# Performance work log

Measured on AMD Instinct MI355X. Metric: run time of the kernel, lower is better.

The kernel has to match this reference:

```python
import jax, jax.numpy as jnp
import numpy as np

EPS = 1e-6
ROPE_BASE = 10000.0


def rmsnorm(x, w):
    xf = x.astype(jnp.float32)
    var = jnp.mean(xf * xf, axis=-1, keepdims=True)
    return (w * (xf * jax.lax.rsqrt(var + EPS))).astype(x.dtype)


def rotate_half(x):
    h = x.shape[-1] // 2
    return jnp.concatenate([-x[..., h:], x[..., :h]], axis=-1)


def setup_inputs() -> dict:
    key = jax.random.key(0)
    ks = jax.random.split(key, 10)
    B, S, H, nH, nKV, hd, I = 2, 2048, 2048, 16, 4, 128, 8192
    hidden_states = jax.random.normal(ks[0], (B, S, H), dtype=jnp.float32)
    # additive causal mask, broadcast over batch/heads
    causal = jnp.triu(jnp.full((S, S), -1e9, dtype=jnp.float32), k=1)
    attention_mask = causal[None, None]  # [1,1,S,S]
    position_ids = jnp.broadcast_to(jnp.arange(S, dtype=jnp.int64), (B, S))
    s = 0.02
    return {
        'hidden_states': hidden_states,
        'attention_mask': attention_mask,
        'position_ids': position_ids,
        'ln1_w': jnp.ones((H,), jnp.float32),
        'Wq': jax.random.normal(ks[1], (H, nH * hd), jnp.float32) * s,
        'Wk': jax.random.normal(ks[2], (H, nKV * hd), jnp.float32) * s,
        'Wv': jax.random.normal(ks[3], (H, nKV * hd), jnp.float32) * s,
        'Wo': jax.random.normal(ks[4], (nH * hd, H), jnp.float32) * s,
        'qn_w': jnp.ones((hd,), jnp.float32),
        'kn_w': jnp.ones((hd,), jnp.float32),
        'ln2_w': jnp.ones((H,), jnp.float32),
        'Wg': jax.random.normal(ks[5], (H, I), jnp.float32) * s,
        'Wu': jax.random.normal(ks[6], (H, I), jnp.float32) * s,
        'Wd': jax.random.normal(ks[7], (I, H), jnp.float32) * s,
    }


def reference(hidden_states, attention_mask, position_ids, ln1_w, Wq, Wk, Wv, Wo,
              qn_w, kn_w, ln2_w, Wg, Wu, Wd):
    B, S, H = hidden_states.shape
    hd = qn_w.shape[0]
    nH = Wq.shape[1] // hd
    nKV = Wk.shape[1] // hd

    # --- attention block ---
    h = rmsnorm(hidden_states, ln1_w)
    q = (h @ Wq).reshape(B, S, nH, hd).transpose(0, 2, 1, 3)   # [B,nH,S,hd]
    k = (h @ Wk).reshape(B, S, nKV, hd).transpose(0, 2, 1, 3)  # [B,nKV,S,hd]
    v = (h @ Wv).reshape(B, S, nKV, hd).transpose(0, 2, 1, 3)

    # RoPE cache (fp32), gathered by position_ids
    inv_freq = 1.0 / (ROPE_BASE ** (jnp.arange(0, hd, 2, dtype=jnp.float32) / hd))
    freqs = jnp.outer(jnp.arange(S, dtype=jnp.float32), inv_freq)
    emb = jnp.concatenate([freqs, freqs], axis=-1)  # [S,hd]
    cos = jnp.cos(emb)[position_ids][:, None]  # [B,1,S,hd]
    sin = jnp.sin(emb)[position_ids][:, None]
    q = q * cos + rotate_half(q) * sin
    k = k * cos + rotate_half(k) * sin

    # QK RMSNorm after RoPE
    q = rmsnorm(q, qn_w)
    k = rmsnorm(k, kn_w)

    # GQA broadcast
    rep = nH // nKV
    k = jnp.repeat(k, rep, axis=1)
    v = jnp.repeat(v, rep, axis=1)

    scores = jnp.einsum('bhqd,bhkd->bhqk', q, k) / np.float32(np.sqrt(hd))
    scores = scores + attention_mask
    attn = jax.nn.softmax(scores.astype(jnp.float32), axis=-1).astype(q.dtype)
    out = jnp.einsum('bhqk,bhkd->bhqd', attn, v)
    out = out.transpose(0, 2, 1, 3).reshape(B, S, nH * hd)
    x = hidden_states + out @ Wo

    # --- MLP block (SwiGLU) ---
    h2 = rmsnorm(x, ln2_w)
    x = x + (jax.nn.silu(h2 @ Wg) * (h2 @ Wu)) @ Wd
    return x
```

## Files before the change

kernel.cpp:

```cpp
#include <hip/hip_runtime.h>
#include <math.h>

typedef __bf16 bf16;
typedef bf16 bf16x8 __attribute__((ext_vector_type(8)));
typedef float f32x4 __attribute__((ext_vector_type(4)));
typedef unsigned int uint32;

#define B_   2
#define S_   2048
#define H_   2048
#define NH_  16
#define NKV_ 4
#define HD_  128
#define I_   8192
#define M_   (B_ * S_)

typedef __attribute__((address_space(3))) void       lds_void;
typedef __attribute__((address_space(1))) const void gbl_void;

__device__ __forceinline__ void async16(const void* g, void* l) {
  __builtin_amdgcn_global_load_lds((gbl_void*)g, (lds_void*)l, 16, 0, 0);
}

__global__ void probe_k(const uint32* __restrict__ x, int* __restrict__ flag) {
  const int lane = threadIdx.x;
  const uint32 u = x[lane];
  float blo = fabsf(__uint_as_float(u << 16));
  float bhi = fabsf(__uint_as_float(u & 0xffff0000u));
  float fv  = fabsf(__uint_as_float(u));
  if (!(blo < 1e30f)) blo = 3e38f;
  if (!(bhi < 1e30f)) bhi = 3e38f;
  if (!(fv  < 1e30f)) fv  = 3e38f;
  float mb = fmaxf(blo, bhi);
  float mf = fv;
#pragma unroll
  for (int off = 1; off < 64; off <<= 1) {
    mb = fmaxf(mb, __shfl_xor(mb, off, 64));
    mf = fmaxf(mf, __shfl_xor(mf, off, 64));
  }
  if (lane == 0) *flag = (mf < mb) ? 1 : 0;
}

template <bool INRAW>
__global__ __launch_bounds__(256) void rmsnorm_k(const void* __restrict__ xin,
                                                 const void* __restrict__ w,
                                                 bf16* __restrict__ out,
                                                 const int* __restrict__ dtp) {
  const int f    = *dtp;
  const int row  = blockIdx.x;
  const int tid  = threadIdx.x;
  const int base = row * H_ + tid * 8;

  float v[8];
  if (INRAW && f) {
    const float* xf = (const float*)xin + base;
    f32x4 a = *(const f32x4*)xf, b = *(const f32x4*)(xf + 4);
#pragma unroll
    for (int i = 0; i < 4; ++i) { v[i] = a[i]; v[4 + i] = b[i]; }
  } else {
    bf16x8 t = *(const bf16x8*)((const bf16*)xin + base);
#pragma unroll
    for (int i = 0; i < 8; ++i) v[i] = (float)t[i];
  }

  float ss = 0.f;
#pragma unroll
  for (int i = 0; i < 8; ++i) ss += v[i] * v[i];
#pragma unroll
  for (int off = 1; off < 64; off <<= 1) ss += __shfl_xor(ss, off, 64);

  __shared__ float red[4];
  if ((tid & 63) == 0) red[tid >> 6] = ss;
  __syncthreads();
  ss = red[0] + red[1] + red[2] + red[3];

  const float scale = rsqrtf(ss * (1.0f / H_) + 1e-6f);
  float wv[8];
  if (f) {
    const float* wf = (const float*)w + tid * 8;
    f32x4 a = *(const f32x4*)wf, b = *(const f32x4*)(wf + 4);
#pragma unroll
    for (int i = 0; i < 4; ++i) { wv[i] = a[i]; wv[4 + i] = b[i]; }
  } else {
    bf16x8 t = *(const bf16x8*)((const bf16*)w + tid * 8);
#pragma unroll
    for (int i = 0; i < 8; ++i) wv[i] = (float)t[i];
  }
  bf16x8 o;
#pragma unroll
  for (int i = 0; i < 8; ++i) o[i] = (bf16)(wv[i] * (v[i] * scale));
  *(bf16x8*)(out + base) = o;
}

__global__ __launch_bounds__(256) void convert_wt(const void* __restrict__ W,
                                                  bf16* __restrict__ Wt,
                                                  const int K, const int N,
                                                  const int* __restrict__ dtp) {
  __shared__ bf16 sT[64][72];
  const int f   = *dtp;
  const int tid = threadIdx.x;
  const int k0  = blockIdx.y * 64;
  const int n0  = blockIdx.x * 64;
  if (f) {
#pragma unroll
    for (int p = 0; p < 4; ++p) {
      const int g  = tid + p * 256;
      const int r  = g >> 4;
      const int c4 = (g & 15) * 4;
      f32x4 v = *(const f32x4*)((const float*)W + (size_t)(k0 + r) * N + n0 + c4);
#pragma unroll
      for (int u = 0; u < 4; ++u) sT[c4 + u][r] = (bf16)v[u];
    }
  } else {
#pragma unroll
    for (int p = 0; p < 2; ++p) {
      const int g  = tid + p * 256;
      const int r  = g >> 3;
      const int c8 = (g & 7) * 8;
      bf16x8 v = *(const bf16x8*)((const bf16*)W + (size_t)(k0 + r) * N + n0 + c8);
#pragma unroll
      for (int u = 0; u < 8; ++u) sT[c8 + u][r] = v[u];
    }
  }
  __syncthreads();
#pragma unroll
  for (int p = 0; p < 2; ++p) {
    const int g  = tid + p * 256;
    const int n  = g >> 3;
    const int k8 = (g & 7) * 8;
    bf16x8 ov;
#pragma unroll
    for (int u = 0; u < 8; ++u) ov[u] = sT[n][k8 + u];
    *(bf16x8*)(Wt + (size_t)(n0 + n) * K + k0 + k8) = ov;
  }
}

#define BARX() do { asm volatile("" ::: "memory");                       \
                    __builtin_amdgcn_s_barrier();                        \
                    asm volatile("" ::: "memory"); } while (0)
#define VMW6() asm volatile("s_waitcnt vmcnt(6)" ::: "memory")

template <int EPI, bool AUXRAW, bool CRAW>
__global__ __launch_bounds__(512, 2) void gemm8_k(const bf16* __restrict__ A,
                                                  const bf16* __restrict__ Bt,
                                                  void* __restrict__ C,
                                                  const void* __restrict__ aux,
                                                  const int M, const int N,
                                                  const int K,
                                                  const int* __restrict__ dtp) {
  __shared__ __align__(16) bf16 sA[2][256][64];
  __shared__ __align__(16) bf16 sB[2][256][64];

  const int f    = *dtp;
  const int tid  = threadIdx.x;
  const int lane = tid & 63;
  const int wave = tid >> 6;
  const int wr   = wave >> 2;
  const int wc   = wave & 3;
  const int l15  = lane & 15;
  const int quad = lane >> 4;

  const int gx  = gridDim.x;
  const int nwg = gx * gridDim.y;
  int bid = blockIdx.y * gx + blockIdx.x;
  if ((nwg & 7) == 0) bid = (bid & 7) * (nwg >> 3) + (bid >> 3);
  const int row0 = (bid / gx) * 256;
  const int col0 = (bid % gx) * 256;

  const int NT = K >> 6;

  const int swo = (l15 & 7) << 4;
  const int cb0 = (quad * 16) ^ swo;
  const int cb1 = (64 + quad * 16) ^ swo;
  char* sAc = (char*)&sA[0][0][0];
  char* sBc = (char*)&sB[0][0][0];

  const int d0   = tid * 16;
  const int d1   = 8192 + tid * 16;
  const int p0   = d0 ^ (((d0 >> 7) & 7) << 4);
  const int p1   = d1 ^ (((d1 >> 7) & 7) << 4);
  const int rg0  = p0 >> 7, cbs0 = p0 & 127;
  const int rg1  = p1 >> 7, cbs1 = p1 & 127;
  const size_t K2 = (size_t)K * 2;
  const char* gA = (const char*)A  + (size_t)row0 * K2;
  const char* gB = (const char*)Bt + (size_t)col0 * K2;

#define STAGE8(gbase, sbase, s, h, t) do {                                     \
    const int tt_ = ((t) < NT) ? (t) : ((t) - NT);                             \
    const size_t go_ = (size_t)tt_ * 128;                                      \
    async16(gbase + (size_t)((h) * 128 + rg0) * K2 + go_ + cbs0,               \
            (sbase) + (s) * 32768 + (h) * 16384 + tid * 16);                   \
    async16(gbase + (size_t)((h) * 128 + rg1) * K2 + go_ + cbs1,               \
            (sbase) + (s) * 32768 + (h) * 16384 + 8192 + tid * 16);            \
  } while (0)
#define STA(s, h, t) STAGE8(gA, sAc, s, h, t)
#define STB(s, h, t) STAGE8(gB, sBc, s, h, t)

  bf16x8 af[4][2], bfr[2][2];
  f32x4 acc[8][4];
#pragma unroll
  for (int m = 0; m < 8; ++m)
#pragma unroll
    for (int n = 0; n < 4; ++n)
#pragma unroll
      for (int r = 0; r < 4; ++r) acc[m][n][r] = 0.f;

#define LDA8(s, mh) do {                                                       \
    _Pragma("unroll")                                                          \
    for (int mi = 0; mi < 4; ++mi) {                                           \
      const int rb = ((mh) * 128 + wr * 64 + mi * 16 + l15) * 128;             \
      af[mi][0] = *(const bf16x8*)(sAc + (s) * 32768 + rb + cb0);              \
      af[mi][1] = *(const bf16x8*)(sAc + (s) * 32768 + rb + cb1);              \
    }                                                                          \
  } while (0)

#define LDB8(s, nh) do {                                                       \
    _Pragma("unroll")                                                          \
    for (int ni = 0; ni < 2; ++ni) {                                           \
      const int rb = ((nh) * 128 + wc * 32 + ni * 16 + l15) * 128;             \
      bfr[ni][0] = *(const bf16x8*)(sBc + (s) * 32768 + rb + cb0);             \
      bfr[ni][1] = *(const bf16x8*)(sBc + (s) * 32768 + rb + cb1);             \
    }                                                                          \
  } while (0)

#define MFMA16(mh, nh) do {                                                    \
    __builtin_amdgcn_s_setprio(1);                                             \
    _Pragma("unroll")                                                          \
    for (int mi = 0; mi < 4; ++mi)                                             \
      _Pragma("unroll")                                                        \
      for (int ni = 0; ni < 2; ++ni) {                                         \
        acc[(mh)*4+mi][(nh)*2+ni] = __builtin_amdgcn_mfma_f32_16x16x32_bf16(   \
            af[mi][0], bfr[ni][0], acc[(mh)*4+mi][(nh)*2+ni], 0, 0, 0);        \
        acc[(mh)*4+mi][(nh)*2+ni] = __builtin_amdgcn_mfma_f32_16x16x32_bf16(   \
            af[mi][1], bfr[ni][1], acc[(mh)*4+mi][(nh)*2+ni], 0, 0, 0);        \
      }                                                                        \
    __builtin_amdgcn_s_setprio(0);                                             \
  } while (0)

  STA(0, 0, 0); STA(0, 1, 0); STB(0, 0, 0); STB(0, 1, 0);
  STA(1, 0, 1); STA(1, 1, 1); STB(1, 0, 1);
  VMW6();
  BARX();

#pragma unroll 1
  for (int T = 0; T < NT; T += 2) {
    LDA8(0, 0); LDB8(0, 0);
    STB(1, 1, T + 1);
    BARX(); MFMA16(0, 0); BARX();
    LDB8(0, 1);
    STA(0, 0, T + 2);
    BARX(); MFMA16(0, 1); BARX();
    LDA8(0, 1); LDB8(0, 0);
    BARX(); MFMA16(1, 0); BARX();
    LDB8(0, 1);
    STA(0, 1, T + 2); STB(0, 0, T + 2);
    BARX(); MFMA16(1, 1); VMW6(); BARX();
    LDA8(1, 0); LDB8(1, 0);
    STB(0, 1, T + 2);
    BARX(); MFMA16(0, 0); BARX();
    LDB8(1, 1);
    STA(1, 0, T + 3);
    BARX(); MFMA16(0, 1); BARX();
    LDA8(1, 1); LDB8(1, 0);
    BARX(); MFMA16(1, 0); BARX();
    LDB8(1, 1);
    STA(1, 1, T + 3); STB(1, 0, T + 3);
    BARX(); MFMA16(1, 1); VMW6(); BARX();
  }
  asm volatile("s_waitcnt vmcnt(0)" ::: "memory");

#pragma unroll
  for (int m = 0; m < 8; ++m) {
#pragma unroll
    for (int n = 0; n < 4; ++n) {
#pragma unroll
      for (int r = 0; r < 4; ++r) {
        const int row = row0 + (m >> 2) * 128 + wr * 64 + (m & 3) * 16 + quad * 4 + r;
        const int col = col0 + (n >> 1) * 128 + wc * 32 + (n & 1) * 16 + l15;
        const size_t idx = (size_t)row * N + col;
        const float val  = acc[m][n][r];
        float outv;
        if (EPI == 0) {
          outv = val;
        } else {
          const float av = (AUXRAW && f) ? ((const float*)aux)[idx]
                                         : (float)((const bf16*)aux)[idx];
          if (EPI == 1) {
            outv = val + av;
          } else {
            const float sg = av / (1.f + __expf(-av));
            outv = sg * val;
          }
        }
        if (CRAW && f) ((float*)C)[idx] = outv;
        else           ((bf16*)C)[idx]  = (bf16)outv;
      }
    }
  }
#undef STAGE8
#undef STA
#undef STB
#undef LDA8
#undef LDB8
#undef MFMA16
}

template <int EPI, bool AUXRAW, bool CRAW>
__global__ __launch_bounds__(256) void gemm_bt_k(const bf16* __restrict__ A,
                                                 const bf16* __restrict__ Bt,
                                                 void* __restrict__ C,
                                                 const void* __restrict__ aux,
                                                 const int M, const int N, const int K,
                                                 const int* __restrict__ dtp) {
  __shared__ __align__(16) bf16 sA[128][32];
  __shared__ __align__(16) bf16 sB[128][32];

  const int f    = *dtp;
  const int tid  = threadIdx.x;
  const int lane = tid & 63;
  const int wave = tid >> 6;
  const int wm   = (wave >> 1) * 64;
  const int wn   = (wave & 1) * 64;
  const int row0 = blockIdx.y * 128;
  const int col0 = blockIdx.x * 128;
  const int l15  = lane & 15;
  const int quad = lane >> 4;

  f32x4 acc[4][4];
#pragma unroll
  for (int i = 0; i < 4; ++i)
#pragma unroll
    for (int j = 0; j < 4; ++j)
#pragma unroll
      for (int r = 0; r < 4; ++r) acc[i][j][r] = 0.f;

  const int o  = tid * 16;
  const int r0 = o >> 6;
  const int ib = o & 63;

  const char* gA0 = (const char*)(A  + (size_t)(row0 + r0)      * K) + ib;
  const char* gA1 = (const char*)(A  + (size_t)(row0 + 64 + r0) * K) + ib;
  const char* gB0 = (const char*)(Bt + (size_t)(col0 + r0)      * K) + ib;
  const char* gB1 = (const char*)(Bt + (size_t)(col0 + 64 + r0) * K) + ib;
  char* lA = (char*)(&sA[0][0]) + wave * 1024;
  char* lB = (char*)(&sB[0][0]) + wave * 1024;

  for (int k0 = 0; k0 < K; k0 += 32) {
    async16(gA0, lA);
    async16(gA1, lA + 4096);
    async16(gB0, lB);
    async16(gB1, lB + 4096);
    gA0 += 64; gA1 += 64; gB0 += 64; gB1 += 64;
    __syncthreads();

    bf16x8 af[4], bfr[4];
#pragma unroll
    for (int i = 0; i < 4; ++i)
      af[i] = *(const bf16x8*)(&sA[wm + i * 16 + l15][quad * 8]);
#pragma unroll
    for (int j = 0; j < 4; ++j)
      bfr[j] = *(const bf16x8*)(&sB[wn + j * 16 + l15][quad * 8]);
#pragma unroll
    for (int i = 0; i < 4; ++i)
#pragma unroll
      for (int j = 0; j < 4; ++j)
        acc[i][j] = __builtin_amdgcn_mfma_f32_16x16x32_bf16(af[i], bfr[j],
                                                            acc[i][j], 0, 0, 0);
    __syncthreads();
  }

#pragma unroll
  for (int i = 0; i < 4; ++i) {
#pragma unroll
    for (int j = 0; j < 4; ++j) {
#pragma unroll
      for (int r = 0; r < 4; ++r) {
        const int row    = row0 + wm + i * 16 + quad * 4 + r;
        const int col    = col0 + wn + j * 16 + l15;
        const size_t idx = (size_t)row * N + col;
        const float val  = acc[i][j][r];
        float outv;
        if (EPI == 0) {
          outv = val;
        } else {
          const float av = (AUXRAW && f) ? ((const float*)aux)[idx]
                                         : (float)((const bf16*)aux)[idx];
          if (EPI == 1) {
            outv = val + av;
          } else {
            const float sg = av / (1.f + __expf(-av));
            outv = sg * val;
          }
        }
        if (CRAW && f) ((float*)C)[idx] = outv;
        else           ((bf16*)C)[idx]  = (bf16)outv;
      }
    }
  }
}

template <int EPI, bool AUXRAW, bool CRAW>
__global__ __launch_bounds__(256) void gemm_k(const bf16* __restrict__ A,
                                              const void* __restrict__ Bm,
                                              void* __restrict__ C,
                                              const void* __restrict__ aux,
                                              const int M, const int N, const int K,
                                              const int* __restrict__ dtp) {
  __shared__ __align__(16) bf16 sA[128][40];
  __shared__ __align__(16) bf16 sB[128][40];

  const int f    = *dtp;
  const int tid  = threadIdx.x;
  const int lane = tid & 63;
  const int wave = tid >> 6;
  const int wm   = (wave >> 1) * 64;
  const int wn   = (wave & 1) * 64;
  const int row0 = blockIdx.y * 128;
  const int col0 = blockIdx.x * 128;
  const int l15  = lane & 15;
  const int quad = lane >> 4;

  f32x4 acc[4][4];
#pragma unroll
  for (int i = 0; i < 4; ++i)
#pragma unroll
    for (int j = 0; j < 4; ++j)
#pragma unroll
      for (int r = 0; r < 4; ++r) acc[i][j][r] = 0.f;

  for (int k0 = 0; k0 < K; k0 += 32) {
#pragma unroll
    for (int pass = 0; pass < 2; ++pass) {
      const int g  = tid + pass * 256;
      const int ar = g >> 2, ac = (g & 3) * 8;
      *(bf16x8*)(&sA[ar][ac]) =
          *(const bf16x8*)(A + (size_t)(row0 + ar) * K + k0 + ac);
      const int br = g >> 4, bc = (g & 15) * 8;
      const size_t boff = (size_t)(k0 + br) * N + col0 + bc;
      bf16x8 bv;
      if (f) {
        const float* bp = (const float*)Bm + boff;
        f32x4 lo = *(const f32x4*)bp, hi = *(const f32x4*)(bp + 4);
#pragma unroll
        for (int u = 0; u < 8; ++u) bv[u] = (bf16)(u < 4 ? lo[u] : hi[u - 4]);
      } else {
        bv = *(const bf16x8*)((const bf16*)Bm + boff);
      }
#pragma unroll
      for (int u = 0; u < 8; ++u) sB[bc + u][br] = bv[u];
    }
    __syncthreads();

    bf16x8 af[4], bfr[4];
#pragma unroll
    for (int i = 0; i < 4; ++i)
      af[i] = *(const bf16x8*)(&sA[wm + i * 16 + l15][quad * 8]);
#pragma unroll
    for (int j = 0; j < 4; ++j)
      bfr[j] = *(const bf16x8*)(&sB[wn + j * 16 + l15][quad * 8]);
#pragma unroll
    for (int i = 0; i < 4; ++i)
#pragma unroll
      for (int j = 0; j < 4; ++j)
        acc[i][j] = __builtin_amdgcn_mfma_f32_16x16x32_bf16(af[i], bfr[j],
                                                            acc[i][j], 0, 0, 0);
    __syncthreads();
  }

#pragma unroll
  for (int i = 0; i < 4; ++i) {
#pragma unroll
    for (int j = 0; j < 4; ++j) {
#pragma unroll
      for (int r = 0; r < 4; ++r) {
        const int row    = row0 + wm + i * 16 + quad * 4 + r;
        const int col    = col0 + wn + j * 16 + l15;
        const size_t idx = (size_t)row * N + col;
        const float val  = acc[i][j][r];
        float outv;
        if (EPI == 0) {
          outv = val;
        } else {
          const float av = (AUXRAW && f) ? ((const float*)aux)[idx]
                                         : (float)((const bf16*)aux)[idx];
          if (EPI == 1) {
            outv = val + av;
          } else {
            const float sg = av / (1.f + __expf(-av));
            outv = sg * val;
          }
        }
        if (CRAW && f) ((float*)C)[idx] = outv;
        else           ((bf16*)C)[idx]  = (bf16)outv;
      }
    }
  }
}

__global__ __launch_bounds__(256) void rope_norm_k(bf16* __restrict__ q,
                                                   bf16* __restrict__ k,
                                                   const void* __restrict__ qw,
                                                   const void* __restrict__ kw,
                                                   const int* __restrict__ dtp) {
  const int f    = *dtp;
  const int task = blockIdx.x * 4 + (threadIdx.x >> 6);
  const int lane = threadIdx.x & 63;
  const int row  = task / 20;
  const int hh   = task - row * 20;

  bf16* p;
  const void* w;
  if (hh < NH_) { p = q + (size_t)row * 2048 + hh * 128;        w = qw; }
  else          { p = k + (size_t)row * 512 + (hh - NH_) * 128; w = kw; }

  const float pos = (float)(row & (S_ - 1));
  const float inv = powf(10000.f, -(float)lane * (1.f / 64.f));
  float sn, cs;
  sincosf(pos * inv, &sn, &cs);

  const float x0 = (float)p[lane], x1 = (float)p[lane + 64];
  const float r0 = x0 * cs - x1 * sn;
  const float r1 = x1 * cs + x0 * sn;

  float ss = r0 * r0 + r1 * r1;
#pragma unroll
  for (int off = 1; off < 64; off <<= 1) ss += __shfl_xor(ss, off, 64);
  const float scale = rsqrtf(ss * (1.f / 128.f) + 1e-6f);

  const float w0 = f ? ((const float*)w)[lane]      : (float)((const bf16*)w)[lane];
  const float w1 = f ? ((const float*)w)[lane + 64] : (float)((const bf16*)w)[lane + 64];
  p[lane]      = (bf16)(w0 * (r0 * scale));
  p[lane + 64] = (bf16)(w1 * (r1 * scale));
}

__global__ __launch_bounds__(256) void transpose_v(const bf16* __restrict__ v,
                                                   bf16* __restrict__ vt) {
  __shared__ bf16 sT[64][68];
  const int tid = threadIdx.x;
  const int r0  = blockIdx.y * 64;
  const int c0  = blockIdx.x * 64;
  const int b   = r0 >> 11;
  const int s0  = r0 & 2047;
#pragma unroll
  for (int p = 0; p < 2; ++p) {
    const int g   = tid + p * 256;
    const int row = g >> 3;
    const int c8  = (g & 7) * 8;
    bf16x8 tv = *(const bf16x8*)(v + (size_t)(r0 + row) * 512 + c0 + c8);
#pragma unroll
    for (int u = 0; u < 8; ++u) sT[c8 + u][row] = tv[u];
  }
  __syncthreads();
#pragma unroll
  for (int p = 0; p < 2; ++p) {
    const int g  = tid + p * 256;
    const int oc = g >> 3;
    const int s8 = (g & 7) * 8;
    bf16x8 ov;
#pragma unroll
    for (int u = 0; u < 8; ++u) ov[u] = sT[oc][s8 + u];
    *(bf16x8*)(vt + ((size_t)(b * 512 + c0 + oc)) * 2048 + s0 + s8) = ov;
  }
}

__global__ __launch_bounds__(256) void attn_mfma(const bf16* __restrict__ q,
                                                 const bf16* __restrict__ k,
                                                 const bf16* __restrict__ vt,
                                                 bf16* __restrict__ ctx) {
  __shared__ __align__(16) bf16 sK[64][136];
  __shared__ __align__(16) bf16 sV[128][72];
  __shared__ __align__(16) bf16 sP[4][16][72];

  const int tid  = threadIdx.x;
  const int lane = tid & 63;
  const int wave = tid >> 6;
  const int l15  = lane & 15;
  const int quad = lane >> 4;

  const int bid = blockIdx.x;
  const int i7  = bid & 127;
  const int qt  = (i7 & 1) ? (127 - (i7 >> 1)) : (i7 >> 1);
  const int kvh = (bid >> 7) & 3;
  const int b   = bid >> 9;
  const int q0  = qt * 16;
  const int h   = kvh * 4 + wave;

  bf16x8 qf[4];
  {
    const bf16* qp = q + (size_t)(b * S_ + q0 + l15) * 2048 + h * 128 + quad * 8;
#pragma unroll
    for (int c = 0; c < 4; ++c) qf[c] = *(const bf16x8*)(qp + c * 32);
  }

  float m4[4], l4[4];
  f32x4 of[8];
#pragma unroll
  for (int r = 0; r < 4; ++r) { m4[r] = -1e30f; l4[r] = 0.f; }
#pragma unroll
  for (int dg = 0; dg < 8; ++dg)
#pragma unroll
    for (int r = 0; r < 4; ++r) of[dg][r] = 0.f;

  const int ntiles = (q0 + 16 + 63) >> 6;
  const bf16* kbase = k + (size_t)b * S_ * 512 + kvh * 128;
  const bf16* vbase = vt + (size_t)(b * 512 + kvh * 128) * 2048;
  const float sc = 0.088388347648318447f;

  for (int t = 0; t < ntiles; ++t) {
    const int j0 = t << 6;
#pragma unroll
    for (int p = 0; p < 4; ++p) {
      const int g   = tid + p * 256;
      const int dc  = g & 15;
      const int key = g >> 4;
      *(bf16x8*)(&sK[key][dc * 8]) =
          *(const bf16x8*)(kbase + (size_t)(j0 + key) * 512 + dc * 8);
    }
#pragma unroll
    for (int p = 0; p < 4; ++p) {
      const int g   = tid + p * 256;
      const int dim = g >> 3;
      const int k8  = (g & 7) * 8;
      *(bf16x8*)(&sV[dim][k8]) =
          *(const bf16x8*)(vbase + (size_t)dim * 2048 + j0 + k8);
    }
    __syncthreads();

    f32x4 sa[4];
#pragma unroll
    for (int g = 0; g < 4; ++g)
#pragma unroll
      for (int r = 0; r < 4; ++r) sa[g][r] = 0.f;
#pragma unroll
    for (int g = 0; g < 4; ++g)
#pragma unroll
      for (int c = 0; c < 4; ++c) {
        bf16x8 kf = *(const bf16x8*)(&sK[g * 16 + l15][c * 32 + quad * 8]);
        sa[g] = __builtin_amdgcn_mfma_f32_16x16x32_bf16(qf[c], kf, sa[g], 0, 0, 0);
      }

    float s[4][4];
    const bool mask = (t == ntiles - 1);
#pragma unroll
    for (int g = 0; g < 4; ++g)
#pragma unroll
      for (int r = 0; r < 4; ++r) {
        float x = sa[g][r] * sc;
        if (mask && (j0 + g * 16 + l15 > q0 + quad * 4 + r)) x = -1e30f;
        s[g][r] = x;
      }

    float al[4];
#pragma unroll
    for (int r = 0; r < 4; ++r) {
      float rm = fmaxf(fmaxf(s[0][r], s[1][r]), fmaxf(s[2][r], s[3][r]));
#pragma unroll
      for (int off = 1; off < 16; off <<= 1) rm = fmaxf(rm, __shfl_xor(rm, off, 64));
      const float mn = fmaxf(m4[r], rm);
      al[r] = __expf(m4[r] - mn);
      float rs = 0.f;
#pragma unroll
      for (int g = 0; g < 4; ++g) { s[g][r] = __expf(s[g][r] - mn); rs += s[g][r]; }
#pragma unroll
      for (int off = 1; off < 16; off <<= 1) rs += __shfl_xor(rs, off, 64);
      l4[r] = l4[r] * al[r] + rs;
      m4[r] = mn;
    }
#pragma unroll
    for (int dg = 0; dg < 8; ++dg)
#pragma unroll
      for (int r = 0; r < 4; ++r) of[dg][r] *= al[r];

#pragma unroll
    for (int g = 0; g < 4; ++g)
#pragma unroll
      for (int r = 0; r < 4; ++r)
        sP[wave][quad * 4 + r][g * 16 + l15] = (bf16)s[g][r];
    bf16x8 pf[2];
#pragma unroll
    for (int c = 0; c < 2; ++c)
      pf[c] = *(const bf16x8*)(&sP[wave][l15][c * 32 + quad * 8]);

#pragma unroll
    for (int c = 0; c < 2; ++c)
#pragma unroll
      for (int dg = 0; dg < 8; ++dg) {
        bf16x8 vf = *(const bf16x8*)(&sV[dg * 16 + l15][c * 32 + quad * 8]);
        of[dg] = __builtin_amdgcn_mfma_f32_16x16x32_bf16(pf[c], vf, of[dg], 0, 0, 0);
      }
    __syncthreads();
  }

  bf16* op = ctx + (size_t)(b * S_ + q0) * 2048 + h * 128;
#pragma unroll
  for (int r = 0; r < 4; ++r) {
    const float rl = 1.f / l4[r];
    const int row  = quad * 4 + r;
#pragma unroll
    for (int dg = 0; dg < 8; ++dg)
      op[(size_t)row * 2048 + dg * 16 + l15] = (bf16)(of[dg][r] * rl);
  }
}

extern "C" void kernel_launch(void* const* d_in, const int* in_sizes, int n_in,
                              void* d_out, int out_size, void* d_ws, size_t ws_size,
                              hipStream_t stream) {
  (void)in_sizes; (void)n_in; (void)out_size;

  const void* hidden = d_in[0];
  const void* ln1 = d_in[3];
  const void* Wq  = d_in[4];
  const void* Wk  = d_in[5];
  const void* Wv  = d_in[6];
  const void* Wo  = d_in[7];
  const void* qn  = d_in[8];
  const void* kn  = d_in[9];
  const void* ln2 = d_in[10];
  const void* Wg  = d_in[11];
  const void* Wu  = d_in[12];
  const void* Wd  = d_in[13];

  int*  dtp   = (int*)d_ws;
  bf16* slotA = (bf16*)((char*)d_ws + 16);
  bf16* slotB = slotA + (size_t)M_ * 2048;
  bf16* slotC = slotB + (size_t)M_ * 2048;
  bf16* slotD = slotC + (size_t)M_ * 512;
  bf16* slotE = slotD + (size_t)M_ * 512;
  bf16* vT    = slotE;
  bf16* wT    = slotE + (size_t)M_ * 8192;

  const size_t need = 16 + 2ull * ((size_t)M_ * 2048 * 2 + (size_t)M_ * 512 * 2 +
                                   (size_t)M_ * 8192 + (size_t)I_ * H_);

  probe_k<<<1, 64, 0, stream>>>((const uint32*)hidden, dtp);
  rmsnorm_k<true><<<M_, 256, 0, stream>>>(hidden, ln1, slotA, dtp);

  if (ws_size >= need) {
    convert_wt<<<dim3(32, 32), 256, 0, stream>>>(Wq, wT, 2048, 2048, dtp);
    gemm8_k<0, false, false><<<dim3(8, 16), 512, 0, stream>>>(slotA, wT, slotB, nullptr, M_, 2048, 2048, dtp);
    convert_wt<<<dim3(8, 32), 256, 0, stream>>>(Wk, wT, 2048, 512, dtp);
    gemm_bt_k<0, false, false><<<dim3(4, 32), 256, 0, stream>>>(slotA, wT, slotC, nullptr, M_, 512, 2048, dtp);
    convert_wt<<<dim3(8, 32), 256, 0, stream>>>(Wv, wT, 2048, 512, dtp);
    gemm_bt_k<0, false, false><<<dim3(4, 32), 256, 0, stream>>>(slotA, wT, slotD, nullptr, M_, 512, 2048, dtp);
    transpose_v<<<dim3(8, 64), 256, 0, stream>>>(slotD, vT);
    rope_norm_k<<<(M_ * (NH_ + NKV_)) / 4, 256, 0, stream>>>(slotB, slotC, qn, kn, dtp);
    attn_mfma<<<B_ * NKV_ * (S_ / 16), 256, 0, stream>>>(slotB, slotC, vT, slotA);
    convert_wt<<<dim3(32, 32), 256, 0, stream>>>(Wo, wT, 2048, 2048, dtp);
    gemm8_k<1, true, false><<<dim3(8, 16), 512, 0, stream>>>(slotA, wT, slotB, hidden, M_, 2048, 2048, dtp);
    rmsnorm_k<false><<<M_, 256, 0, stream>>>(slotB, ln2, slotA, dtp);
    convert_wt<<<dim3(128, 32), 256, 0, stream>>>(Wg, wT, 2048, 8192, dtp);
    gemm8_k<0, false, false><<<dim3(32, 16), 512, 0, stream>>>(slotA, wT, slotE, nullptr, M_, 8192, 2048, dtp);
    convert_wt<<<dim3(128, 32), 256, 0, stream>>>(Wu, wT, 2048, 8192, dtp);
    gemm8_k<2, false, false><<<dim3(32, 16), 512, 0, stream>>>(slotA, wT, slotE, slotE, M_, 8192, 2048, dtp);
    convert_wt<<<dim3(32, 128), 256, 0, stream>>>(Wd, wT, 8192, 2048, dtp);
    gemm8_k<1, false, true><<<dim3(8, 16), 512, 0, stream>>>(slotE, wT, d_out, slotB, M_, 2048, 8192, dtp);
  } else {
    gemm_k<0, false, false><<<dim3(16, 32), 256, 0, stream>>>(slotA, Wq, slotB, nullptr, M_, 2048, 2048, dtp);
    gemm_k<0, false, false><<<dim3(4, 32), 256, 0, stream>>>(slotA, Wk, slotC, nullptr, M_, 512, 2048, dtp);
    gemm_k<0, false, false><<<dim3(4, 32), 256, 0, stream>>>(slotA, Wv, slotD, nullptr, M_, 512, 2048, dtp);
    transpose_v<<<dim3(8, 64), 256, 0, stream>>>(slotD, vT);
    rope_norm_k<<<(M_ * (NH_ + NKV_)) / 4, 256, 0, stream>>>(slotB, slotC, qn, kn, dtp);
    attn_mfma<<<B_ * NKV_ * (S_ / 16), 256, 0, stream>>>(slotB, slotC, vT, slotA);
    gemm_k<1, true, false><<<dim3(16, 32), 256, 0, stream>>>(slotA, Wo, slotB, hidden, M_, 2048, 2048, dtp);
    rmsnorm_k<false><<<M_, 256, 0, stream>>>(slotB, ln2, slotA, dtp);
    gemm_k<0, false, false><<<dim3(64, 32), 256, 0, stream>>>(slotA, Wg, slotE, nullptr, M_, 8192, 2048, dtp);
    gemm_k<2, false, false><<<dim3(64, 32), 256, 0, stream>>>(slotA, Wu, slotE, slotE, M_, 8192, 2048, dtp);
    gemm_k<1, false, true><<<dim3(16, 32), 256, 0, stream>>>(slotE, Wd, d_out, slotB, M_, 2048, 8192, dtp);
  }
}
```

Measured before the change: 1.420 ms.

## Split-K the narrow GEMMs into two partials and add a combine kernel

The Q/K/V, O and down-projection GEMMs now run with split-K across blockIdx.z. Each half writes fp32 partials to extra workspace, and a new combine kernel sums the halves and applies the residual/epilogue. This doubles the workgroup count for the 128-tile GEMMs, which underfill the GPU, at the cost of extra fp32 partial traffic and additional launches. The gemm8 barrier macro also drops its compiler fences, and an explicit lgkmcnt(0) wait with a sched_barrier is added before each MFMA block. The new path only runs when the workspace is large enough; otherwise the previous path is kept.

```diff
diff --git a/kernel.cpp b/kernel.cpp
--- a/kernel.cpp
+++ b/kernel.cpp
@@ -3,6 +3,7 @@
 
 typedef __bf16 bf16;
 typedef bf16 bf16x8 __attribute__((ext_vector_type(8)));
+typedef bf16 bf16x4 __attribute__((ext_vector_type(4)));
 typedef float f32x4 __attribute__((ext_vector_type(4)));
 typedef unsigned int uint32;
 
@@ -135,10 +136,58 @@
   }
 }
 
-#define BARX() do { asm volatile("" ::: "memory");                       \
-                    __builtin_amdgcn_s_barrier();                        \
-                    asm volatile("" ::: "memory"); } while (0)
-#define VMW6() asm volatile("s_waitcnt vmcnt(6)" ::: "memory")
+template <int EPI, bool AUXRAW, bool CRAW>
+__global__ __launch_bounds__(256) void combine_k(const float* __restrict__ p0,
+                                                 const float* __restrict__ p1,
+                                                 const void* __restrict__ aux,
+                                                 void* __restrict__ C,
+                                                 const size_t total,
+                                                 const int* __restrict__ dtp) {
+  const int f = *dtp;
+  const size_t i = ((size_t)blockIdx.x * 256 + threadIdx.x) * 4;
+  if (i >= total) return;
+  f32x4 a = *(const f32x4*)(p0 + i);
+  f32x4 b = *(const f32x4*)(p1 + i);
+  float av4[4];
+  if (EPI != 0) {
+    if (AUXRAW && f) {
+      f32x4 t = *(const f32x4*)((const float*)aux + i);
+#pragma unroll
+      for (int u = 0; u < 4; ++u) av4[u] = t[u];
+    } else {
+      bf16x4 t = *(const bf16x4*)((const bf16*)aux + i);
+#pragma unroll
+      for (int u = 0; u < 4; ++u) av4[u] = (float)t[u];
+    }
+  }
+  float o[4];
+#pragma unroll
+  for (int u = 0; u < 4; ++u) {
+    const float val = a[u] + b[u];
+    if (EPI == 0) o[u] = val;
+    else if (EPI == 1) o[u] = val + av4[u];
+    else {
+      const float sg = av4[u] / (1.f + __expf(-av4[u]));
+      o[u] = sg * val;
+    }
+  }
+  if (CRAW && f) {
+    f32x4 ov; 
+#pragma unroll
+    for (int u = 0; u < 4; ++u) ov[u] = o[u];
+    *(f32x4*)((float*)C + i) = ov;
+  } else {
+    bf16x4 ov;
+#pragma unroll
+    for (int u = 0; u < 4; ++u) ov[u] = (bf16)o[u];
+    *(bf16x4*)((bf16*)C + i) = ov;
+  }
+}
+
+#define BARX()  __builtin_amdgcn_s_barrier()
+#define LGKM0() do { asm volatile("s_waitcnt lgkmcnt(0)" ::: "memory");       \
+                     __builtin_amdgcn_sched_barrier(0); } while (0)
+#define VMW6()  asm volatile("s_waitcnt vmcnt(6)" ::: "memory")
 
 template <int EPI, bool AUXRAW, bool CRAW>
 __global__ __launch_bounds__(512, 2) void gemm8_k(const bf16* __restrict__ A,
@@ -146,7 +195,7 @@
                                                   void* __restrict__ C,
                                                   const void* __restrict__ aux,
                                                   const int M, const int N,
-                                                  const int K,
+                                                  const int K, const int lda,
                                                   const int* __restrict__ dtp) {
   __shared__ __align__(16) bf16 sA[2][256][64];
   __shared__ __align__(16) bf16 sB[2][256][64];
@@ -166,6 +215,7 @@
   if ((nwg & 7) == 0) bid = (bid & 7) * (nwg >> 3) + (bid >> 3);
   const int row0 = (bid / gx) * 256;
   const int col0 = (bid % gx) * 256;
+  const int koff = blockIdx.z * K;
 
   const int NT = K >> 6;
 
@@ -181,16 +231,16 @@
   const int p1   = d1 ^ (((d1 >> 7) & 7) << 4);
   const int rg0  = p0 >> 7, cbs0 = p0 & 127;
   const int rg1  = p1 >> 7, cbs1 = p1 & 127;
-  const size_t K2 = (size_t)K * 2;
-  const char* gA = (const char*)A  + (size_t)row0 * K2;
-  const char* gB = (const char*)Bt + (size_t)col0 * K2;
+  const size_t LD2 = (size_t)lda * 2;
+  const char* gA = (const char*)A  + (size_t)row0 * LD2 + (size_t)koff * 2;
+  const char* gB = (const char*)Bt + (size_t)col0 * LD2 + (size_t)koff * 2;
 
 #define STAGE8(gbase, sbase, s, h, t) do {                                     \
     const int tt_ = ((t) < NT) ? (t) : ((t) - NT);                             \
     const size_t go_ = (size_t)tt_ * 128;                                      \
-    async16(gbase + (size_t)((h) * 128 + rg0) * K2 + go_ + cbs0,               \
+    async16(gbase + (size_t)((h) * 128 + rg0) * LD2 + go_ + cbs0,              \
             (sbase) + (s) * 32768 + (h) * 16384 + tid * 16);                   \
-    async16(gbase + (size_t)((h) * 128 + rg1) * K2 + go_ + cbs1,               \
+    async16(gbase + (size_t)((h) * 128 + rg1) * LD2 + go_ + cbs1,              \
             (sbase) + (s) * 32768 + (h) * 16384 + 8192 + tid * 16);            \
   } while (0)
 #define STA(s, h, t) STAGE8(gA, sAc, s, h, t)
@@ -246,29 +296,31 @@
   for (int T = 0; T < NT; T += 2) {
     LDA8(0, 0); LDB8(0, 0);
     STB(1, 1, T + 1);
-    BARX(); MFMA16(0, 0); BARX();
+    BARX(); LGKM0(); MFMA16(0, 0); BARX();
     LDB8(0, 1);
     STA(0, 0, T + 2);
-    BARX(); MFMA16(0, 1); BARX();
+    BARX(); LGKM0(); MFMA16(0, 1); BARX();
     LDA8(0, 1); LDB8(0, 0);
-    BARX(); MFMA16(1, 0); BARX();
+    BARX(); LGKM0(); MFMA16(1, 0); BARX();
     LDB8(0, 1);
     STA(0, 1, T + 2); STB(0, 0, T + 2);
-    BARX(); MFMA16(1, 1); VMW6(); BARX();
+    BARX(); LGKM0(); MFMA16(1, 1); VMW6(); BARX();
     LDA8(1, 0); LDB8(1, 0);
     STB(0, 1, T + 2);
-    BARX(); MFMA16(0, 0); BARX();
+    BARX(); LGKM0(); MFMA16(0, 0); BARX();
     LDB8(1, 1);
     STA(1, 0, T + 3);
-    BARX(); MFMA16(0, 1); BARX();
+    BARX(); LGKM0(); MFMA16(0, 1); BARX();
     LDA8(1, 1); LDB8(1, 0);
-    BARX(); MFMA16(1, 0); BARX();
+    BARX(); LGKM0(); MFMA16(1, 0); BARX();
     LDB8(1, 1);
     STA(1, 1, T + 3); STB(1, 0, T + 3);
-    BARX(); MFMA16(1, 1); VMW6(); BARX();
+    BARX(); LGKM0(); MFMA16(1, 1); VMW6(); BARX();
   }
   asm volatile("s_waitcnt vmcnt(0)" ::: "memory");
 
+  float* P = (EPI == 3)
+      ? (float*)C + (size_t)blockIdx.z * ((size_t)M * N) : nullptr;
 #pragma unroll
   for (int m = 0; m < 8; ++m) {
 #pragma unroll
@@ -279,21 +331,25 @@
         const int col = col0 + (n >> 1) * 128 + wc * 32 + (n & 1) * 16 + l15;
         const size_t idx = (size_t)row * N + col;
         const float val  = acc[m][n][r];
-        float outv;
-        if (EPI == 0) {
-          outv = val;
+        if (EPI == 3) {
+          P[idx] = val;
         } else {
-          const float av = (AUXRAW && f) ? ((const float*)aux)[idx]
-                                         : (float)((const bf16*)aux)[idx];
-          if (EPI == 1) {
-            outv = val + av;
+          float outv;
+          if (EPI == 0) {
+            outv = val;
           } else {
-            const float sg = av / (1.f + __expf(-av));
-            outv = sg * val;
+            const float av = (AUXRAW && f) ? ((const float*)aux)[idx]
+                                           : (float)((const bf16*)aux)[idx];
+            if (EPI == 1) {
+              outv = val + av;
+            } else {
+              const float sg = av / (1.f + __expf(-av));
+              outv = sg * val;
+            }
           }
+          if (CRAW && f) ((float*)C)[idx] = outv;
+          else           ((bf16*)C)[idx]  = (bf16)outv;
         }
-        if (CRAW && f) ((float*)C)[idx] = outv;
-        else           ((bf16*)C)[idx]  = (bf16)outv;
       }
     }
   }
@@ -310,10 +366,112 @@
                                                  const bf16* __restrict__ Bt,
                                                  void* __restrict__ C,
                                                  const void* __restrict__ aux,
-                                                 const int M, const int N, const int K,
+                                                 const int M, const int N,
+                                                 const int K, const int lda,
                                                  const int* __restrict__ dtp) {
   __shared__ __align__(16) bf16 sA[128][32];
   __shared__ __align__(16) bf16 sB[128][32];
+
+  const int f    = *dtp;
+  const int tid  = threadIdx.x;
+  const int lane = tid & 63;
+  const int wave = tid >> 6;
+  const int wm   = (wave >> 1) * 64;
+  const int wn   = (wave & 1) * 64;
+  const int row0 = blockIdx.y * 128;
+  const int col0 = blockIdx.x * 128;
+  const int koff = blockIdx.z * K;
+  const int l15  = lane & 15;
+  const int quad = lane >> 4;
+
+  f32x4 acc[4][4];
+#pragma unroll
+  for (int i = 0; i < 4; ++i)
+#pragma unroll
+    for (int j = 0; j < 4; ++j)
+#pragma unroll
+      for (int r = 0; r < 4; ++r) acc[i][j][r] = 0.f;
+
+  const int o  = tid * 16;
+  const int r0 = o >> 6;
+  const int ib = o & 63;
+
+  const char* gA0 = (const char*)(A  + (size_t)(row0 + r0)      * lda + koff) + ib;
+  const char* gA1 = (const char*)(A  + (size_t)(row0 + 64 + r0) * lda + koff) + ib;
+  const char* gB0 = (const char*)(Bt + (size_t)(col0 + r0)      * lda + koff) + ib;
+  const char* gB1 = (const char*)(Bt + (size_t)(col0 + 64 + r0) * lda + koff) + ib;
+  char* lA = (char*)(&sA[0][0]) + wave * 1024;
+  char* lB = (char*)(&sB[0][0]) + wave * 1024;
+
+  for (int k0 = 0; k0 < K; k0 += 32) {
+    async16(gA0, lA);
+    async16(gA1, lA + 4096);
+    async16(gB0, lB);
+    async16(gB1, lB + 4096);
+    gA0 += 64; gA1 += 64; gB0 += 64; gB1 += 64;
+    __syncthreads();
+
+    bf16x8 af[4], bfr[4];
+#pragma unroll
+    for (int i = 0; i < 4; ++i)
+      af[i] = *(const bf16x8*)(&sA[wm + i * 16 + l15][quad * 8]);
+#pragma unroll
+    for (int j = 0; j < 4; ++j)
+      bfr[j] = *(const bf16x8*)(&sB[wn + j * 16 + l15][quad * 8]);
+#pragma unroll
+    for (int i = 0; i < 4; ++i)
+#pragma unroll
+      for (int j = 0; j < 4; ++j)
+        acc[i][j] = __builtin_amdgcn_mfma_f32_16x16x32_bf16(af[i], bfr[j],
+                                                            acc[i][j], 0, 0, 0);
+    __syncthreads();
+  }
+
+  float* P = (EPI == 3)
+      ? (float*)C + (size_t)blockIdx.z * ((size_t)M * N) : nullptr;
+#pragma unroll
+  for (int i = 0; i < 4; ++i) {
+#pragma unroll
+    for (int j = 0; j < 4; ++j) {
+#pragma unroll
+      for (int r = 0; r < 4; ++r) {
+        const int row    = row0 + wm + i * 16 + quad * 4 + r;
+        const int col    = col0 + wn + j * 16 + l15;
+        const size_t idx = (size_t)row * N + col;
+        const float val  = acc[i][j][r];
+        if (EPI == 3) {
+          P[idx] = val;
+        } else {
+          float outv;
+          if (EPI == 0) {
+            outv = val;
+          } else {
+            const float av = (AUXRAW && f) ? ((const float*)aux)[idx]
+                                           : (float)((const bf16*)aux)[idx];
+            if (EPI == 1) {
+              outv = val + av;
+            } else {
+              const float sg = av / (1.f + __expf(-av));
+              outv = sg * val;
+            }
+          }
+          if (CRAW && f) ((float*)C)[idx] = outv;
+          else           ((bf16*)C)[idx]  = (bf16)outv;
+        }
+      }
+    }
+  }
+}
+
+template <int EPI, bool AUXRAW, bool CRAW>
+__global__ __launch_bounds__(256) void gemm_k(const bf16* __restrict__ A,
+                                              const void* __restrict__ Bm,
+                                              void* __restrict__ C,
+                                              const void* __restrict__ aux,
+                                              const int M, const int N, const int K,
+                                              const int* __restrict__ dtp) {
+  __shared__ __align__(16) bf16 sA[128][40];
+  __shared__ __align__(16) bf16 sB[128][40];
 
   const int f    = *dtp;
   const int tid  = threadIdx.x;
@@ -334,23 +492,27 @@
 #pragma unroll
       for (int r = 0; r < 4; ++r) acc[i][j][r] = 0.f;
 
-  const int o  = tid * 16;
-  const int r0 = o >> 6;
-  const int ib = o & 63;
-
-  const char* gA0 = (const char*)(A  + (size_t)(row0 + r0)      * K) + ib;
-  const char* gA1 = (const char*)(A  + (size_t)(row0 + 64 + r0) * K) + ib;
-  const char* gB0 = (const char*)(Bt + (size_t)(col0 + r0)      * K) + ib;
-  const char* gB1 = (const char*)(Bt + (size_t)(col0 + 64 + r0) * K) + ib;
-  char* lA = (char*)(&sA[0][0]) + wave * 1024;
-  char* lB = (char*)(&sB[0][0]) + wave * 1024;
-
   for (int k0 = 0; k0 < K; k0 += 32) {
-    async16(gA0, lA);
-    async16(gA1, lA + 4096);
-    async16(gB0, lB);
-    async16(gB1, lB + 4096);
-    gA0 += 64; gA1 += 64; gB0 += 64; gB1 += 64;
+#pragma unroll
+    for (int pass = 0; pass < 2; ++pass) {
+      const int g  = tid + pass * 256;
+      const int ar = g >> 2, ac = (g & 3) * 8;
+      *(bf16x8*)(&sA[ar][ac]) =
+          *(const bf16x8*)(A + (size_t)(row0 + ar) * K + k0 + ac);
+      const int br = g >> 4, bc = (g & 15) * 8;
+      const size_t boff = (size_t)(k0 + br) * N + col0 + bc;
+      bf16x8 bv;
+      if (f) {
+        const float* bp = (const float*)Bm + boff;
+        f32x4 lo = *(const f32x4*)bp, hi = *(const f32x4*)(bp + 4);
+#pragma unroll
+        for (int u = 0; u < 8; ++u) bv[u] = (bf16)(u < 4 ? lo[u] : hi[u - 4]);
+      } else {
+        bv = *(const bf16x8*)((const bf16*)Bm + boff);
+      }
+#pragma unroll
+      for (int u = 0; u < 8; ++u) sB[bc + u][br] = bv[u];
+    }
     __syncthreads();
 
     bf16x8 af[4], bfr[4];
@@ -399,104 +561,6 @@
   }
 }
 
-template <int EPI, bool AUXRAW, bool CRAW>
-__global__ __launch_bounds__(256) void gemm_k(const bf16* __restrict__ A,
-                                              const void* __restrict__ Bm,
-                                              void* __restrict__ C,
-                                              const void* __restrict__ aux,
-                                              const int M, const int N, const int K,
-                                              const int* __restrict__ dtp) {
-  __shared__ __align__(16) bf16 sA[128][40];
-  __shared__ __align__(16) bf16 sB[128][40];
-
-  const int f    = *dtp;
-  const int tid  = threadIdx.x;
-  const int lane = tid & 63;
-  const int wave = tid >> 6;
-  const int wm   = (wave >> 1) * 64;
-  const int wn   = (wave & 1) * 64;
-  const int row0 = blockIdx.y * 128;
-  const int col0 = blockIdx.x * 128;
-  const int l15  = lane & 15;
-  const int quad = lane >> 4;
-
-  f32x4 acc[4][4];
-#pragma unroll
-  for (int i = 0; i < 4; ++i)
-#pragma unroll
-    for (int j = 0; j < 4; ++j)
-#pragma unroll
-      for (int r = 0; r < 4; ++r) acc[i][j][r] = 0.f;
-
-  for (int k0 = 0; k0 < K; k0 += 32) {
-#pragma unroll
-    for (int pass = 0; pass < 2; ++pass) {
-      const int g  = tid + pass * 256;
-      const int ar = g >> 2, ac = (g & 3) * 8;
-      *(bf16x8*)(&sA[ar][ac]) =
-          *(const bf16x8*)(A + (size_t)(row0 + ar) * K + k0 + ac);
-      const int br = g >> 4, bc = (g & 15) * 8;
-      const size_t boff = (size_t)(k0 + br) * N + col0 + bc;
-      bf16x8 bv;
-      if (f) {
-        const float* bp = (const float*)Bm + boff;
-        f32x4 lo = *(const f32x4*)bp, hi = *(const f32x4*)(bp + 4);
-#pragma unroll
-        for (int u = 0; u < 8; ++u) bv[u] = (bf16)(u < 4 ? lo[u] : hi[u - 4]);
-      } else {
-        bv = *(const bf16x8*)((const bf16*)Bm + boff);
-      }
-#pragma unroll
-      for (int u = 0; u < 8; ++u) sB[bc + u][br] = bv[u];
-    }
-    __syncthreads();
-
-    bf16x8 af[4], bfr[4];
-#pragma unroll
-    for (int i = 0; i < 4; ++i)
-      af[i] = *(const bf16x8*)(&sA[wm + i * 16 + l15][quad * 8]);
-#pragma unroll
-    for (int j = 0; j < 4; ++j)
-      bfr[j] = *(const bf16x8*)(&sB[wn + j * 16 + l15][quad * 8]);
-#pragma unroll
-    for (int i = 0; i < 4; ++i)
-#pragma unroll
-      for (int j = 0; j < 4; ++j)
-        acc[i][j] = __builtin_amdgcn_mfma_f32_16x16x32_bf16(af[i], bfr[j],
-                                                            acc[i][j], 0, 0, 0);
-    __syncthreads();
-  }
-
-#pragma unroll
-  for (int i = 0; i < 4; ++i) {
-#pragma unroll
-    for (int j = 0; j < 4; ++j) {
-#pragma unroll
-      for (int r = 0; r < 4; ++r) {
-        const int row    = row0 + wm + i * 16 + quad * 4 + r;
-        const int col    = col0 + wn + j * 16 + l15;
-        const size_t idx = (size_t)row * N + col;
-        const float val  = acc[i][j][r];
-        float outv;
-        if (EPI == 0) {
-          outv = val;
-        } else {
-          const float av = (AUXRAW && f) ? ((const float*)aux)[idx]
-                                         : (float)((const bf16*)aux)[idx];
-          if (EPI == 1) {
-            outv = val + av;
-          } else {
-            const float sg = av / (1.f + __expf(-av));
-            outv = sg * val;
-          }
-        }
-        if (CRAW && f) ((float*)C)[idx] = outv;
-        else           ((bf16*)C)[idx]  = (bf16)outv;
-      }
-    }
-  }
-}
-
 __global__ __launch_bounds__(256) void rope_norm_k(bf16* __restrict__ q,
                                                    bf16* __restrict__ k,
                                                    const void* __restrict__ qw,
@@ -728,32 +792,59 @@
   bf16* slotE = slotD + (size_t)M_ * 512;
   bf16* vT    = slotE;
   bf16* wT    = slotE + (size_t)M_ * 8192;
-
-  const size_t need = 16 + 2ull * ((size_t)M_ * 2048 * 2 + (size_t)M_ * 512 * 2 +
-                                   (size_t)M_ * 8192 + (size_t)I_ * H_);
+  float* pP   = (float*)(wT + (size_t)I_ * H_);
+  float* pP1  = pP + (size_t)M_ * 2048;
+
+  const size_t need1 = 16 + 2ull * ((size_t)M_ * 2048 * 2 + (size_t)M_ * 512 * 2 +
+                                    (size_t)M_ * 8192 + (size_t)I_ * H_);
+  const size_t need2 = need1 + 2ull * (size_t)M_ * 2048 * 4;
 
   probe_k<<<1, 64, 0, stream>>>((const uint32*)hidden, dtp);
   rmsnorm_k<true><<<M_, 256, 0, stream>>>(hidden, ln1, slotA, dtp);
 
-  if (ws_size >= need) {
+  if (ws_size >= need2) {
     convert_wt<<<dim3(32, 32), 256, 0, stream>>>(Wq, wT, 2048, 2048, dtp);
-    gemm8_k<0, false, false><<<dim3(8, 16), 512, 0, stream>>>(slotA, wT, slotB, nullptr, M_, 2048, 2048, dtp);
+    gemm8_k<3, false, false><<<dim3(8, 16, 2), 512, 0, stream>>>(slotA, wT, pP, nullptr, M_, 2048, 1024, 2048, dtp);
+    combine_k<0, false, false><<<(M_ * 2048) / 1024, 256, 0, stream>>>(pP, pP1, nullptr, slotB, (size_t)M_ * 2048, dtp);
     convert_wt<<<dim3(8, 32), 256, 0, stream>>>(Wk, wT, 2048, 512, dtp);
-    gemm_bt_k<0, false, false><<<dim3(4, 32), 256, 0, stream>>>(slotA, wT, slotC, nullptr, M_, 512, 2048, dtp);
+    gemm_bt_k<3, false, false><<<dim3(4, 32, 2), 256, 0, stream>>>(slotA, wT, pP, nullptr, M_, 512, 1024, 2048, dtp);
+    combine_k<0, false, false><<<(M_ * 512) / 1024, 256, 0, stream>>>(pP, pP + (size_t)M_ * 512, nullptr, slotC, (size_t)M_ * 512, dtp);
     convert_wt<<<dim3(8, 32), 256, 0, stream>>>(Wv, wT, 2048, 512, dtp);
-    gemm_bt_k<0, false, false><<<dim3(4, 32), 256, 0, stream>>>(slotA, wT, slotD, nullptr, M_, 512, 2048, dtp);
+    gemm_bt_k<3, false, false><<<dim3(4, 32, 2), 256, 0, stream>>>(slotA, wT, pP, nullptr, M_, 512, 1024, 2048, dtp);
+    combine_k<0, false, false><<<(M_ * 512) / 1024, 256, 0, stream>>>(pP, pP + (size_t)M_ * 512, nullptr, slotD, (size_t)M_ * 512, dtp);
     transpose_v<<<dim3(8, 64), 256, 0, stream>>>(slotD, vT);
     rope_norm_k<<<(M_ * (NH_ + NKV_)) / 4, 256, 0, stream>>>(slotB, slotC, qn, kn, dtp);
     attn_mfma<<<B_ * NKV_ * (S_ / 16), 256, 0, stream>>>(slotB, slotC, vT, slotA);
     convert_wt<<<dim3(32, 32), 256, 0, stream>>>(Wo, wT, 2048, 2048, dtp);
-    gemm8_k<1, true, false><<<dim3(8, 16), 512, 0, stream>>>(slotA, wT, slotB, hidden, M_, 2048, 2048, dtp);
+    gemm8_k<3, false, false><<<dim3(8, 16, 2), 512, 0, stream>>>(slotA, wT, pP, nullptr, M_, 2048, 1024, 2048, dtp);
+    combine_k<1, true, false><<<(M_ * 2048) / 1024, 256, 0, stream>>>(pP, pP1, hidden, slotB, (size_t)M_ * 2048, dtp);
     rmsnorm_k<false><<<M_, 256, 0, stream>>>(slotB, ln2, slotA, dtp);
     convert_wt<<<dim3(128, 32), 256, 0, stream>>>(Wg, wT, 2048, 8192, dtp);
-    gemm8_k<0, false, false><<<dim3(32, 16), 512, 0, stream>>>(slotA, wT, slotE, nullptr, M_, 8192, 2048, dtp);
+    gemm8_k<0, false, false><<<dim3(32, 16), 512, 0, stream>>>(slotA, wT, slotE, nullptr, M_, 8192, 2048, 2048, dtp);
     convert_wt<<<dim3(128, 32), 256, 0, stream>>>(Wu, wT, 2048, 8192, dtp);
-    gemm8_k<2, false, false><<<dim3(32, 16), 512, 0, stream>>>(slotA, wT, slotE, slotE, M_, 8192, 2048, dtp);
+    gemm8_k<2, false, false><<<dim3(32, 16), 512, 0, stream>>>(slotA, wT, slotE, slotE, M_, 8192, 2048, 2048, dtp);
     convert_wt<<<dim3(32, 128), 256, 0, stream>>>(Wd, wT, 8192, 2048, dtp);
-    gemm8_k<1, false, true><<<dim3(8, 16), 512, 0, stream>>>(slotE, wT, d_out, slotB, M_, 2048, 8192, dtp);
+    gemm8_k<3, false, false><<<dim3(8, 16, 2), 512, 0, stream>>>(slotE, wT, pP, nullptr, M_, 2048, 4096, 8192, dtp);
+    combine_k<1, false, true><<<(M_ * 2048) / 1024, 256, 0, stream>>>(pP, pP1, slotB, d_out, (size_t)M_ * 2048, dtp);
+  } else if (ws_size >= need1) {
+    convert_wt<<<dim3(32, 32), 256, 0, stream>>>(Wq, wT, 2048, 2048, dtp);
+    gemm8_k<0, false, false><<<dim3(8, 16), 512, 0, stream>>>(slotA, wT, slotB, nullptr, M_, 2048, 2048, 2048, dtp);
+    convert_wt<<<dim3(8, 32), 256, 0, stream>>>(Wk, wT, 2048, 512, dtp);
+    gemm_bt_k<0, false, false><<<dim3(4, 32), 256, 0, stream>>>(slotA, wT, slotC, nullptr, M_, 512, 2048, 2048, dtp);
+    convert_wt<<<dim3(8, 32), 256, 0, stream>>>(Wv, wT, 2048, 512, dtp);
+    gemm_bt_k<0, false, false><<<dim3(4, 32), 256, 0, stream>>>(slotA, wT, slotD, nullptr, M_, 512, 2048, 2048, dtp);
+    transpose_v<<<dim3(8, 64), 256, 0, stream>>>(slotD, vT);
+    rope_norm_k<<<(M_ * (NH_ + NKV_)) / 4, 256, 0, stream>>>(slotB, slotC, qn, kn, dtp);
+    attn_mfma<<<B_ * NKV_ * (S_ / 16), 256, 0, stream>>>(slotB, slotC, vT, slotA);
+    convert_wt<<<dim3(32, 32), 256, 0, stream>>>(Wo, wT, 2048, 2048, dtp);
+    gemm8_k<1, true, false><<<dim3(8, 16), 512, 0, stream>>>(slotA, wT, slotB, hidden, M_, 2048, 2048, 2048, dtp);
+    rmsnorm_k<false><<<M_, 256, 0, stream>>>(slotB, ln2, slotA, dtp);
+    convert_wt<<<dim3(128, 32), 256, 0, stream>>>(Wg, wT, 2048, 8192, dtp);
+    gemm8_k<0, false, false><<<dim3(32, 16), 512, 0, stream>>>(slotA, wT, slotE, nullptr, M_, 8192, 2048, 2048, dtp);
+    convert_wt<<<dim3(128, 32), 256, 0, stream>>>(Wu, wT, 2048, 8192, dtp);
+    gemm8_k<2, false, false><<<dim3(32, 16), 512, 0, stream>>>(slotA, wT, slotE, slotE, M_, 8192, 2048, 2048, dtp);
+    convert_wt<<<dim3(32, 128), 256, 0, stream>>>(Wd, wT, 8192, 2048, dtp);
+    gemm8_k<1, false, true><<<dim3(8, 16), 512, 0, stream>>>(slotE, wT, d_out, slotB, M_, 2048, 8192, 8192, dtp);
   } else {
     gemm_k<0, false, false><<<dim3(16, 32), 256, 0, stream>>>(slotA, Wq, slotB, nullptr, M_, 2048, 2048, dtp);
     gemm_k<0, false, false><<<dim3(4, 32), 256, 0, stream>>>(slotA, Wk, slotC, nullptr, M_, 512, 2048, dtp);
```

Result: faster. 1.215 ms, median of 2 (-14.4%).
